# Optimization experiments

Hardware: AMD Instinct MI355X
Metric: run time of the kernel (lower is better)

## Reference

```python
import jax, jax.numpy as jnp
import numpy as np

INPUT_SIZE = 1024
HIDDEN_SIZE = 1024
BATCH = 8192
MLP_H1, MLP_H2 = 16, 8


def _uniform(key, shape, stdv):
    return jax.random.uniform(key, shape, jnp.float32, -stdv, stdv)


def setup_inputs() -> dict:
    key = jax.random.key(0)
    ks = jax.random.split(key, 20)
    stdv = 1.0 / np.sqrt(HIDDEN_SIZE)
    I, H = INPUT_SIZE, HIDDEN_SIZE
    inp = {
        "x": jax.random.normal(ks[0], (BATCH, I), jnp.float32),
        "h": jax.random.normal(ks[1], (BATCH, H), jnp.float32),
        "c": jax.random.normal(ks[2], (BATCH, H), jnp.float32),
        # gate weights (torch layout: matmul(h, W_h*) + matmul(x, W_x*) + b)
        "W_hi": _uniform(ks[3], (H, H), stdv),
        "W_xi": _uniform(ks[4], (I, H), stdv),
        "b_i": _uniform(ks[5], (H,), stdv),
        "W_hc": _uniform(ks[6], (H, H), stdv),
        "W_xc": _uniform(ks[7], (I, H), stdv),
        "b_c": _uniform(ks[8], (H,), stdv),
        "W_ho": _uniform(ks[9], (H, H), stdv),
        "W_xo": _uniform(ks[10], (I, H), stdv),
        "b_o": _uniform(ks[11], (H,), stdv),
        # forget MLP: (I+H) -> 16 -> 8 -> H, ReLU hidden, sigmoid output
        "W1": _uniform(ks[12], (I + H, MLP_H1), stdv),
        "b1": _uniform(ks[13], (MLP_H1,), stdv),
        "W2": _uniform(ks[14], (MLP_H1, MLP_H2), stdv),
        "b2": _uniform(ks[15], (MLP_H2,), stdv),
        "W3": _uniform(ks[16], (MLP_H2, H), stdv),
        "b3": _uniform(ks[17], (H,), stdv),
    }
    return inp


def reference(x, h, c, W_hi, W_xi, b_i, W_hc, W_xc, b_c, W_ho, W_xo, b_o,
              W1, b1, W2, b2, W3, b3):
    # forget gate via small MLP on concat(x, h)
    xh = jnp.concatenate((x, h), axis=1)           # [B, I+H]
    z = jax.nn.relu(xh @ W1 + b1)                  # [B, 16]
    z = jax.nn.relu(z @ W2 + b2)                   # [B, 8]
    f = jax.nn.sigmoid(z @ W3 + b3)                # [B, H]

    i = jax.nn.sigmoid(h @ W_hi + x @ W_xi + b_i)
    g = jnp.tanh(h @ W_hc + x @ W_xc + b_c)
    o = jax.nn.sigmoid(h @ W_ho + x @ W_xo + b_o)

    c_new = f * c + i * g
    h_new = o * jnp.tanh(c_new)
    return (h_new, c_new, f)
```

## Files before the change

### kernel.cpp

```cpp
#include <hip/hip_runtime.h>
#include <math.h>

#define BATCH 8192
#define HDIM  1024
#define KDIM  2048
#define NDIM  3072

typedef __attribute__((ext_vector_type(8))) short short8;
typedef __attribute__((ext_vector_type(4))) float floatx4;

__device__ __forceinline__ float b2f(unsigned short u) {
  union { unsigned int i; float f; } v; v.i = ((unsigned int)u) << 16; return v.f;
}
__device__ __forceinline__ unsigned short f2b(float f) {
  union { unsigned int i; float f; } v; v.f = f;
  unsigned int r = v.i + 0x7FFFu + ((v.i >> 16) & 1u);
  return (unsigned short)(r >> 16);
}
__device__ __forceinline__ float ldsel(const void* p, size_t i, int isbf) {
  return isbf ? b2f(((const unsigned short*)p)[i]) : ((const float*)p)[i];
}
__device__ __forceinline__ float sigf(float x) { return 1.0f / (1.0f + __expf(-x)); }
__device__ __forceinline__ float tanhfast(float x) {
  float a = __builtin_fabsf(x);
  float t = __expf(-2.f * a);
  float r = (1.f - t) / (1.f + t);
  return copysignf(r, x);
}

__device__ __forceinline__ int detect_bf(const void* x) {
  unsigned int w = ((const unsigned int*)x)[threadIdx.x & 63];
  unsigned short lo = (unsigned short)(w & 0xFFFFu);
  int e = (lo >> 7) & 0xFF;
  bool ok = (e >= 110 && e <= 135) || ((lo & 0x7FFFu) == 0);
  unsigned long long m = __ballot(ok);
  return (__popcll(m) >= 48) ? 1 : 0;
}

__device__ __forceinline__ void gld16(const void* g, void* l) {
  auto gp = reinterpret_cast<__attribute__((address_space(1))) unsigned int*>(
      (unsigned long long)g);
  auto lp = reinterpret_cast<__attribute__((address_space(3))) unsigned int*>(
      (unsigned long long)l);
  __builtin_amdgcn_global_load_lds(gp, lp, 16, 0, 0);
}

__device__ __forceinline__ short8 ld8bf(const void* p, size_t off, int isbf) {
  short8 r;
  if (isbf) {
    r = *(const short8*)((const unsigned short*)p + off);
  } else {
    const float* s = (const float*)p + off;
    float4 a = *(const float4*)(s);
    float4 b = *(const float4*)(s + 4);
    r[0]=(short)f2b(a.x); r[1]=(short)f2b(a.y); r[2]=(short)f2b(a.z); r[3]=(short)f2b(a.w);
    r[4]=(short)f2b(b.x); r[5]=(short)f2b(b.y); r[6]=(short)f2b(b.z); r[7]=(short)f2b(b.w);
  }
  return r;
}

__global__ __launch_bounds__(256) void k_prep(
    const void* __restrict__ x, const void* __restrict__ h,
    const void* __restrict__ W1, const void* __restrict__ b1,
    const void* __restrict__ W2, const void* __restrict__ b2,
    unsigned short* __restrict__ A, float* __restrict__ z2) {
  __shared__ __align__(16) unsigned short tA[16 * 256];
  __shared__ __align__(16) unsigned short tB[16 * 256];
  __shared__ float part[4 * 16 * 17];
  __shared__ float z1s[16 * 17];
  const int isbf = detect_bf(x);
  const int tid = threadIdx.x;
  const int m0 = blockIdx.x * 16;
  const int lane = tid & 63;
  const int w = tid >> 6;
  const int q = lane >> 4;
  const int r = lane & 15;
  char* tAb = (char*)tA;
  char* tBb = (char*)tB;

  const int arow = tid >> 4;
  const int ak = (tid & 15) * 16;

  floatx4 acc = {0.f, 0.f, 0.f, 0.f};

  for (int ktile = 0; ktile < 8; ++ktile) {
    const int k0 = ktile * 256;
    const void* src = (k0 < 1024) ? x : h;
    const int klocal = (k0 & 1023) + ak;
    short8 v0 = ld8bf(src, (size_t)(m0 + arow) * 1024 + klocal, isbf);
    short8 v1 = ld8bf(src, (size_t)(m0 + arow) * 1024 + klocal + 8, isbf);
    float wv[16];
    if (isbf) {
      const unsigned short* s = (const unsigned short*)W1 + (size_t)(k0 + tid) * 16;
      short8 s0 = *(const short8*)(s);
      short8 s1 = *(const short8*)(s + 8);
#pragma unroll
      for (int j = 0; j < 8; ++j) { wv[j] = b2f((unsigned short)s0[j]);
                                    wv[8 + j] = b2f((unsigned short)s1[j]); }
    } else {
      const float* s = (const float*)W1 + (size_t)(k0 + tid) * 16;
      float4 a0 = *(const float4*)(s);
      float4 a1 = *(const float4*)(s + 4);
      float4 a2 = *(const float4*)(s + 8);
      float4 a3 = *(const float4*)(s + 12);
      wv[0]=a0.x; wv[1]=a0.y; wv[2]=a0.z; wv[3]=a0.w;
      wv[4]=a1.x; wv[5]=a1.y; wv[6]=a1.z; wv[7]=a1.w;
      wv[8]=a2.x; wv[9]=a2.y; wv[10]=a2.z; wv[11]=a2.w;
      wv[12]=a3.x; wv[13]=a3.y; wv[14]=a3.z; wv[15]=a3.w;
    }
    if (!isbf) {
      unsigned short* Ao = A + (size_t)(m0 + arow) * KDIM + k0 + ak;
      *(short8*)(Ao) = v0;
      *(short8*)(Ao + 8) = v1;
    }
    {
      const int base = arow * 512 + ak * 2;
      const int sw = (arow & 7) << 4;
      *(short8*)(tAb + ((base) ^ sw)) = v0;
      *(short8*)(tAb + ((base + 16) ^ sw)) = v1;
    }
#pragma unroll
    for (int j = 0; j < 16; ++j) {
      *(unsigned short*)(tBb + ((j * 512 + tid * 2) ^ ((j & 7) << 4))) = f2b(wv[j]);
    }
    __syncthreads();
#pragma unroll
    for (int s = 0; s < 2; ++s) {
      const int ks = (w * 2 + s) * 32 + q * 8;
      short8 af = *(const short8*)(tAb + ((r * 512 + ks * 2) ^ ((r & 7) << 4)));
      short8 bf = *(const short8*)(tBb + ((r * 512 + ks * 2) ^ ((r & 7) << 4)));
      acc = __builtin_amdgcn_mfma_f32_16x16x32_bf16(af, bf, acc, 0, 0, 0);
    }
    __syncthreads();
  }
#pragma unroll
  for (int t = 0; t < 4; ++t) part[(w * 16 + q * 4 + t) * 17 + r] = acc[t];
  __syncthreads();
  {
    const int row = tid >> 4;
    const int n = tid & 15;
    float s = part[(0 * 16 + row) * 17 + n] + part[(1 * 16 + row) * 17 + n] +
              part[(2 * 16 + row) * 17 + n] + part[(3 * 16 + row) * 17 + n] +
              ldsel(b1, (size_t)n, isbf);
    z1s[row * 17 + n] = fmaxf(s, 0.f);
  }
  __syncthreads();
  if (tid < 128) {
    const int row = tid >> 3;
    const int p = tid & 7;
    float s = ldsel(b2, (size_t)p, isbf);
#pragma unroll
    for (int nn = 0; nn < 16; ++nn)
      s += z1s[row * 17 + nn] * ldsel(W2, (size_t)nn * 8 + p, isbf);
    z2[(size_t)(m0 + row) * 8 + p] = fmaxf(s, 0.f);
  }
}

__global__ __launch_bounds__(256) void k_wt(
    const void* __restrict__ x,
    const void* __restrict__ wxi, const void* __restrict__ whi,
    const void* __restrict__ wxc, const void* __restrict__ whc,
    const void* __restrict__ wxo, const void* __restrict__ who,
    unsigned short* __restrict__ WT) {
  __shared__ __align__(16) float tbuf[64][65];
  const int isbf = detect_bf(x);
  const int tid = threadIdx.x;
  const int b = blockIdx.x;
  const int mat = b >> 8;
  const int rem = b & 255;
  const int ti = rem >> 4;
  const int tj = rem & 15;
  const void* Ws[6] = {wxi, whi, wxc, whc, wxo, who};
  const void* W = Ws[mat];
  const int gt = mat >> 1;
  const int half = mat & 1;
  const int rrow = tid >> 3;
  const int c8 = (tid & 7) * 8;
#pragma unroll
  for (int it = 0; it < 2; ++it) {
    int row = it * 32 + rrow;
    size_t off = (size_t)(ti * 64 + row) * 1024 + tj * 64 + c8;
    if (isbf) {
      const unsigned short* s = (const unsigned short*)W + off;
      ushort4 a = *(const ushort4*)(s);
      ushort4 bv = *(const ushort4*)(s + 4);
      tbuf[row][c8+0]=b2f(a.x);  tbuf[row][c8+1]=b2f(a.y);
      tbuf[row][c8+2]=b2f(a.z);  tbuf[row][c8+3]=b2f(a.w);
      tbuf[row][c8+4]=b2f(bv.x); tbuf[row][c8+5]=b2f(bv.y);
      tbuf[row][c8+6]=b2f(bv.z); tbuf[row][c8+7]=b2f(bv.w);
    } else {
      const float* s = (const float*)W + off;
      float4 a = *(const float4*)(s);
      float4 bv = *(const float4*)(s + 4);
      tbuf[row][c8+0]=a.x;  tbuf[row][c8+1]=a.y;  tbuf[row][c8+2]=a.z;  tbuf[row][c8+3]=a.w;
      tbuf[row][c8+4]=bv.x; tbuf[row][c8+5]=bv.y; tbuf[row][c8+6]=bv.z; tbuf[row][c8+7]=bv.w;
    }
  }
  __syncthreads();
#pragma unroll
  for (int it = 0; it < 2; ++it) {
    int nl = it * 32 + rrow;
    int n = gt * 1024 + tj * 64 + nl;
    int kk = half * 1024 + ti * 64 + c8;
    short8 pk;
#pragma unroll
    for (int i = 0; i < 8; ++i) pk[i] = (short)f2b(tbuf[c8 + i][nl]);
    *(short8*)(WT + (size_t)n * KDIM + kk) = pk;
  }
}

__global__ __launch_bounds__(256, 3) void k_gemm(
    const void* __restrict__ x, const void* __restrict__ h,
    const unsigned short* __restrict__ Apack,
    const unsigned short* __restrict__ WT,
    unsigned short* __restrict__ P) {
  const int isbf = detect_bf(x);
  const unsigned short* Ax = isbf ? (const unsigned short*)x : Apack;
  const unsigned short* Ah = isbf ? (const unsigned short*)h : (Apack + 1024);
  const int sA = isbf ? 1024 : 2048;
  __shared__ __align__(16) unsigned short lA[128 * 64];
  __shared__ __align__(16) unsigned short lB[128 * 64];
  const int tid = threadIdx.x;
  const int lane = tid & 63;
  const int wv = tid >> 6;
  const int wm = (wv >> 1) << 6;
  const int wn = (wv & 1) << 6;
  const int m0 = blockIdx.y << 7;
  const int n0 = blockIdx.x << 7;

  floatx4 acc[4][4];
  const floatx4 fzero = {0.f, 0.f, 0.f, 0.f};
#pragma unroll
  for (int i = 0; i < 4; ++i)
#pragma unroll
    for (int j = 0; j < 4; ++j) acc[i][j] = fzero;

  int rr[4], kk[4];
#pragma unroll
  for (int ps = 0; ps < 4; ++ps) {
    int chunk = ps * 256 + tid;
    rr[ps] = chunk >> 3;
    kk[ps] = (chunk & 7) ^ (rr[ps] & 7);
  }
  const int px0 = (lane >> 4) ^ (lane & 7);
  const int px1 = ((lane >> 4) + 4) ^ (lane & 7);
  const int rowA = wm + (lane & 15);
  const int rowB = wn + (lane & 15);

  for (int kt = 0; kt < KDIM / 64; ++kt) {
    const int k0 = kt * 64;
    const unsigned short* Abase = (k0 < 1024) ? (Ax + k0) : (Ah + (k0 - 1024));
#pragma unroll
    for (int ps = 0; ps < 4; ++ps) {
      const int chunk = ps * 256 + tid;
      gld16(Abase + (size_t)(m0 + rr[ps]) * sA + kk[ps] * 8, lA + chunk * 8);
      gld16(WT + ((size_t)(n0 + rr[ps]) * KDIM + k0 + kk[ps] * 8), lB + chunk * 8);
    }
    __syncthreads();
#pragma unroll
    for (int s = 0; s < 2; ++s) {
      const int px = s ? px1 : px0;
      short8 af[4], bfr[4];
#pragma unroll
      for (int i = 0; i < 4; ++i)
        af[i] = *(const short8*)(lA + ((((rowA + (i << 4)) << 3) + px) << 3));
#pragma unroll
      for (int i = 0; i < 4; ++i)
        bfr[i] = *(const short8*)(lB + ((((rowB + (i << 4)) << 3) + px) << 3));
#pragma unroll
      for (int mi = 0; mi < 4; ++mi)
#pragma unroll
        for (int ni = 0; ni < 4; ++ni)
          acc[mi][ni] = __builtin_amdgcn_mfma_f32_16x16x32_bf16(
              af[mi], bfr[ni], acc[mi][ni], 0, 0, 0);
    }
    __syncthreads();
  }
  const int col = lane & 15;
  const int rq = (lane >> 4) << 2;
#pragma unroll
  for (int mi = 0; mi < 4; ++mi) {
#pragma unroll
    for (int ni = 0; ni < 4; ++ni) {
      const size_t n = (size_t)(n0 + wn + (ni << 4) + col);
#pragma unroll
      for (int t = 0; t < 4; ++t) {
        const size_t m = (size_t)(m0 + wm + (mi << 4) + rq + t);
        P[m * NDIM + n] = f2b(acc[mi][ni][t]);
      }
    }
  }
}

__global__ __launch_bounds__(256) void k_pointwise(
    const unsigned short* __restrict__ P, const void* __restrict__ x,
    const void* __restrict__ cin,
    const void* __restrict__ bi, const void* __restrict__ bc,
    const void* __restrict__ bo, const float* __restrict__ z2,
    const void* __restrict__ W3, const void* __restrict__ b3,
    void* __restrict__ out) {
  const int isbf = detect_bf(x);
  const int tid = threadIdx.x;
  const int n = tid * 4;
  const size_t MH = (size_t)BATCH * HDIM;

  float w3r[8][4], bif[4], bcf[4], bof[4], b3f[4];
  if (isbf) {
#pragma unroll
    for (int j = 0; j < 8; ++j) {
      ushort4 u = *(const ushort4*)((const unsigned short*)W3 + j * 1024 + n);
      w3r[j][0]=b2f(u.x); w3r[j][1]=b2f(u.y); w3r[j][2]=b2f(u.z); w3r[j][3]=b2f(u.w);
    }
    ushort4 u3 = *(const ushort4*)((const unsigned short*)b3 + n);
    b3f[0]=b2f(u3.x); b3f[1]=b2f(u3.y); b3f[2]=b2f(u3.z); b3f[3]=b2f(u3.w);
    ushort4 a = *(const ushort4*)((const unsigned short*)bi + n);
    ushort4 b = *(const ushort4*)((const unsigned short*)bc + n);
    ushort4 d = *(const ushort4*)((const unsigned short*)bo + n);
    bif[0]=b2f(a.x); bif[1]=b2f(a.y); bif[2]=b2f(a.z); bif[3]=b2f(a.w);
    bcf[0]=b2f(b.x); bcf[1]=b2f(b.y); bcf[2]=b2f(b.z); bcf[3]=b2f(b.w);
    bof[0]=b2f(d.x); bof[1]=b2f(d.y); bof[2]=b2f(d.z); bof[3]=b2f(d.w);
  } else {
#pragma unroll
    for (int j = 0; j < 8; ++j) {
      float4 u = *(const float4*)((const float*)W3 + j * 1024 + n);
      w3r[j][0]=u.x; w3r[j][1]=u.y; w3r[j][2]=u.z; w3r[j][3]=u.w;
    }
    float4 u3 = *(const float4*)((const float*)b3 + n);
    b3f[0]=u3.x; b3f[1]=u3.y; b3f[2]=u3.z; b3f[3]=u3.w;
    float4 a = *(const float4*)((const float*)bi + n);
    float4 b = *(const float4*)((const float*)bc + n);
    float4 d = *(const float4*)((const float*)bo + n);
    bif[0]=a.x; bif[1]=a.y; bif[2]=a.z; bif[3]=a.w;
    bcf[0]=b.x; bcf[1]=b.y; bcf[2]=b.z; bcf[3]=b.w;
    bof[0]=d.x; bof[1]=d.y; bof[2]=d.z; bof[3]=d.w;
  }

  const size_t m0 = (size_t)blockIdx.x * 8;
#pragma unroll
  for (int rI = 0; rI < 8; ++rI) {
    const size_t m = m0 + rI;
    const size_t idx = m * 1024 + n;
    const unsigned short* pr = P + m * NDIM + n;
    ushort4 ui = *(const ushort4*)(pr);
    ushort4 ug = *(const ushort4*)(pr + 1024);
    ushort4 uo = *(const ushort4*)(pr + 2048);
    float pi[4] = {b2f(ui.x), b2f(ui.y), b2f(ui.z), b2f(ui.w)};
    float pg[4] = {b2f(ug.x), b2f(ug.y), b2f(ug.z), b2f(ug.w)};
    float po[4] = {b2f(uo.x), b2f(uo.y), b2f(uo.z), b2f(uo.w)};
    float4 za = *(const float4*)(z2 + m * 8);
    float4 zb = *(const float4*)(z2 + m * 8 + 4);
    float zz[8] = {za.x, za.y, za.z, za.w, zb.x, zb.y, zb.z, zb.w};
    float cf[4];
    if (isbf) {
      ushort4 e = *(const ushort4*)((const unsigned short*)cin + idx);
      cf[0]=b2f(e.x); cf[1]=b2f(e.y); cf[2]=b2f(e.z); cf[3]=b2f(e.w);
    } else {
      float4 e = *(const float4*)((const float*)cin + idx);
      cf[0]=e.x; cf[1]=e.y; cf[2]=e.z; cf[3]=e.w;
    }
    float f3[4] = {b3f[0], b3f[1], b3f[2], b3f[3]};
#pragma unroll
    for (int j = 0; j < 8; ++j) {
      f3[0] += zz[j] * w3r[j][0];
      f3[1] += zz[j] * w3r[j][1];
      f3[2] += zz[j] * w3r[j][2];
      f3[3] += zz[j] * w3r[j][3];
    }
    float hn[4], cn[4], ff[4];
#pragma unroll
    for (int t = 0; t < 4; ++t) {
      float F = sigf(f3[t]);
      float I = sigf(pi[t] + bif[t]);
      float G = tanhfast(pg[t] + bcf[t]);
      float O = sigf(po[t] + bof[t]);
      float C = F * cf[t] + I * G;
      ff[t] = F;
      cn[t] = C;
      hn[t] = O * tanhfast(C);
    }
    if (isbf) {
      unsigned short* ob = (unsigned short*)out;
      *(ushort4*)(ob + idx) = make_ushort4(f2b(hn[0]), f2b(hn[1]), f2b(hn[2]), f2b(hn[3]));
      *(ushort4*)(ob + MH + idx) = make_ushort4(f2b(cn[0]), f2b(cn[1]), f2b(cn[2]), f2b(cn[3]));
      *(ushort4*)(ob + 2 * MH + idx) = make_ushort4(f2b(ff[0]), f2b(ff[1]), f2b(ff[2]), f2b(ff[3]));
    } else {
      float* ob = (float*)out;
      *(float4*)(ob + idx) = make_float4(hn[0], hn[1], hn[2], hn[3]);
      *(float4*)(ob + MH + idx) = make_float4(cn[0], cn[1], cn[2], cn[3]);
      *(float4*)(ob + 2 * MH + idx) = make_float4(ff[0], ff[1], ff[2], ff[3]);
    }
  }
}

extern "C" void kernel_launch(void* const* d_in, const int* in_sizes, int n_in,
                              void* d_out, int out_size, void* d_ws, size_t ws_size,
                              hipStream_t stream) {
  const void* x    = d_in[0];
  const void* h    = d_in[1];
  const void* c    = d_in[2];
  const void* W_hi = d_in[3];
  const void* W_xi = d_in[4];
  const void* b_i  = d_in[5];
  const void* W_hc = d_in[6];
  const void* W_xc = d_in[7];
  const void* b_c  = d_in[8];
  const void* W_ho = d_in[9];
  const void* W_xo = d_in[10];
  const void* b_o  = d_in[11];
  const void* W1   = d_in[12];
  const void* b1   = d_in[13];
  const void* W2   = d_in[14];
  const void* b2   = d_in[15];
  const void* W3   = d_in[16];
  const void* b3   = d_in[17];

  char* ws = (char*)d_ws;
  unsigned short* A   = (unsigned short*)ws;
  unsigned short* WT  = (unsigned short*)(ws + 33554432);
  unsigned short* P   = (unsigned short*)(ws + 46137344);
  float*          z2b = (float*)(ws + 96468992);

  k_prep<<<dim3(512), dim3(256), 0, stream>>>(x, h, W1, b1, W2, b2, A, z2b);
  k_wt<<<dim3(1536), dim3(256), 0, stream>>>(x, W_xi, W_hi, W_xc, W_hc,
                                             W_xo, W_ho, WT);
  k_gemm<<<dim3(NDIM / 128, BATCH / 128), dim3(256), 0, stream>>>(x, h, A, WT, P);
  k_pointwise<<<dim3(BATCH / 8), dim3(256), 0, stream>>>(P, x, c, b_i, b_c, b_o,
                                                         z2b, W3, b3, d_out);
}
```

Baseline: 351.2 us.

## Merge prep and weight-transpose kernels, swizzle GEMM tiles, widen pointwise vectors

Folds the MLP-prep and weight-transpose kernels into one launch, picking the path from the block index, so one launch and its dependency gap go away and the two jobs can share the GPU. Remaps GEMM block indices with a stride swizzle to change which tiles run at the same time, aiming for better L2 reuse. The pointwise kernel now handles 8 columns per thread with 16-byte loads and stores over 4 rows per block, and keeps W3 packed as bf16 in registers. In fp32 mode W3 is rounded to bf16, which adds a small precision loss in the forget gate.

```diff
diff --git a/kernel.cpp b/kernel.cpp
--- a/kernel.cpp
+++ b/kernel.cpp
@@ -59,153 +59,164 @@
   return r;
 }
 
-__global__ __launch_bounds__(256) void k_prep(
+__device__ __forceinline__ void ld8f(const void* p, size_t off, int isbf, float* o) {
+  if (isbf) {
+    short8 s = *(const short8*)((const unsigned short*)p + off);
+#pragma unroll
+    for (int j = 0; j < 8; ++j) o[j] = b2f((unsigned short)s[j]);
+  } else {
+    const float* s = (const float*)p + off;
+    float4 a = *(const float4*)(s);
+    float4 b = *(const float4*)(s + 4);
+    o[0]=a.x; o[1]=a.y; o[2]=a.z; o[3]=a.w;
+    o[4]=b.x; o[5]=b.y; o[6]=b.z; o[7]=b.w;
+  }
+}
+
+__global__ __launch_bounds__(256) void k_pre(
     const void* __restrict__ x, const void* __restrict__ h,
     const void* __restrict__ W1, const void* __restrict__ b1,
     const void* __restrict__ W2, const void* __restrict__ b2,
-    unsigned short* __restrict__ A, float* __restrict__ z2) {
-  __shared__ __align__(16) unsigned short tA[16 * 256];
-  __shared__ __align__(16) unsigned short tB[16 * 256];
-  __shared__ float part[4 * 16 * 17];
-  __shared__ float z1s[16 * 17];
-  const int isbf = detect_bf(x);
-  const int tid = threadIdx.x;
-  const int m0 = blockIdx.x * 16;
-  const int lane = tid & 63;
-  const int w = tid >> 6;
-  const int q = lane >> 4;
-  const int r = lane & 15;
-  char* tAb = (char*)tA;
-  char* tBb = (char*)tB;
-
-  const int arow = tid >> 4;
-  const int ak = (tid & 15) * 16;
-
-  floatx4 acc = {0.f, 0.f, 0.f, 0.f};
-
-  for (int ktile = 0; ktile < 8; ++ktile) {
-    const int k0 = ktile * 256;
-    const void* src = (k0 < 1024) ? x : h;
-    const int klocal = (k0 & 1023) + ak;
-    short8 v0 = ld8bf(src, (size_t)(m0 + arow) * 1024 + klocal, isbf);
-    short8 v1 = ld8bf(src, (size_t)(m0 + arow) * 1024 + klocal + 8, isbf);
-    float wv[16];
-    if (isbf) {
-      const unsigned short* s = (const unsigned short*)W1 + (size_t)(k0 + tid) * 16;
-      short8 s0 = *(const short8*)(s);
-      short8 s1 = *(const short8*)(s + 8);
-#pragma unroll
-      for (int j = 0; j < 8; ++j) { wv[j] = b2f((unsigned short)s0[j]);
-                                    wv[8 + j] = b2f((unsigned short)s1[j]); }
-    } else {
-      const float* s = (const float*)W1 + (size_t)(k0 + tid) * 16;
-      float4 a0 = *(const float4*)(s);
-      float4 a1 = *(const float4*)(s + 4);
-      float4 a2 = *(const float4*)(s + 8);
-      float4 a3 = *(const float4*)(s + 12);
-      wv[0]=a0.x; wv[1]=a0.y; wv[2]=a0.z; wv[3]=a0.w;
-      wv[4]=a1.x; wv[5]=a1.y; wv[6]=a1.z; wv[7]=a1.w;
-      wv[8]=a2.x; wv[9]=a2.y; wv[10]=a2.z; wv[11]=a2.w;
-      wv[12]=a3.x; wv[13]=a3.y; wv[14]=a3.z; wv[15]=a3.w;
-    }
-    if (!isbf) {
-      unsigned short* Ao = A + (size_t)(m0 + arow) * KDIM + k0 + ak;
-      *(short8*)(Ao) = v0;
-      *(short8*)(Ao + 8) = v1;
-    }
-    {
-      const int base = arow * 512 + ak * 2;
-      const int sw = (arow & 7) << 4;
-      *(short8*)(tAb + ((base) ^ sw)) = v0;
-      *(short8*)(tAb + ((base + 16) ^ sw)) = v1;
-    }
-#pragma unroll
-    for (int j = 0; j < 16; ++j) {
-      *(unsigned short*)(tBb + ((j * 512 + tid * 2) ^ ((j & 7) << 4))) = f2b(wv[j]);
-    }
-    __syncthreads();
-#pragma unroll
-    for (int s = 0; s < 2; ++s) {
-      const int ks = (w * 2 + s) * 32 + q * 8;
-      short8 af = *(const short8*)(tAb + ((r * 512 + ks * 2) ^ ((r & 7) << 4)));
-      short8 bf = *(const short8*)(tBb + ((r * 512 + ks * 2) ^ ((r & 7) << 4)));
-      acc = __builtin_amdgcn_mfma_f32_16x16x32_bf16(af, bf, acc, 0, 0, 0);
-    }
-    __syncthreads();
-  }
-#pragma unroll
-  for (int t = 0; t < 4; ++t) part[(w * 16 + q * 4 + t) * 17 + r] = acc[t];
-  __syncthreads();
-  {
-    const int row = tid >> 4;
-    const int n = tid & 15;
-    float s = part[(0 * 16 + row) * 17 + n] + part[(1 * 16 + row) * 17 + n] +
-              part[(2 * 16 + row) * 17 + n] + part[(3 * 16 + row) * 17 + n] +
-              ldsel(b1, (size_t)n, isbf);
-    z1s[row * 17 + n] = fmaxf(s, 0.f);
-  }
-  __syncthreads();
-  if (tid < 128) {
-    const int row = tid >> 3;
-    const int p = tid & 7;
-    float s = ldsel(b2, (size_t)p, isbf);
-#pragma unroll
-    for (int nn = 0; nn < 16; ++nn)
-      s += z1s[row * 17 + nn] * ldsel(W2, (size_t)nn * 8 + p, isbf);
-    z2[(size_t)(m0 + row) * 8 + p] = fmaxf(s, 0.f);
-  }
-}
-
-__global__ __launch_bounds__(256) void k_wt(
-    const void* __restrict__ x,
     const void* __restrict__ wxi, const void* __restrict__ whi,
     const void* __restrict__ wxc, const void* __restrict__ whc,
     const void* __restrict__ wxo, const void* __restrict__ who,
-    unsigned short* __restrict__ WT) {
-  __shared__ __align__(16) float tbuf[64][65];
+    unsigned short* __restrict__ A, unsigned short* __restrict__ WT,
+    float* __restrict__ z2) {
+  __shared__ __align__(16) char smem[21888];
   const int isbf = detect_bf(x);
   const int tid = threadIdx.x;
-  const int b = blockIdx.x;
-  const int mat = b >> 8;
-  const int rem = b & 255;
-  const int ti = rem >> 4;
-  const int tj = rem & 15;
-  const void* Ws[6] = {wxi, whi, wxc, whc, wxo, who};
-  const void* W = Ws[mat];
-  const int gt = mat >> 1;
-  const int half = mat & 1;
-  const int rrow = tid >> 3;
-  const int c8 = (tid & 7) * 8;
-#pragma unroll
-  for (int it = 0; it < 2; ++it) {
-    int row = it * 32 + rrow;
-    size_t off = (size_t)(ti * 64 + row) * 1024 + tj * 64 + c8;
-    if (isbf) {
-      const unsigned short* s = (const unsigned short*)W + off;
-      ushort4 a = *(const ushort4*)(s);
-      ushort4 bv = *(const ushort4*)(s + 4);
-      tbuf[row][c8+0]=b2f(a.x);  tbuf[row][c8+1]=b2f(a.y);
-      tbuf[row][c8+2]=b2f(a.z);  tbuf[row][c8+3]=b2f(a.w);
-      tbuf[row][c8+4]=b2f(bv.x); tbuf[row][c8+5]=b2f(bv.y);
-      tbuf[row][c8+6]=b2f(bv.z); tbuf[row][c8+7]=b2f(bv.w);
-    } else {
-      const float* s = (const float*)W + off;
-      float4 a = *(const float4*)(s);
-      float4 bv = *(const float4*)(s + 4);
-      tbuf[row][c8+0]=a.x;  tbuf[row][c8+1]=a.y;  tbuf[row][c8+2]=a.z;  tbuf[row][c8+3]=a.w;
-      tbuf[row][c8+4]=bv.x; tbuf[row][c8+5]=bv.y; tbuf[row][c8+6]=bv.z; tbuf[row][c8+7]=bv.w;
-    }
-  }
-  __syncthreads();
-#pragma unroll
-  for (int it = 0; it < 2; ++it) {
-    int nl = it * 32 + rrow;
-    int n = gt * 1024 + tj * 64 + nl;
-    int kk = half * 1024 + ti * 64 + c8;
-    short8 pk;
-#pragma unroll
-    for (int i = 0; i < 8; ++i) pk[i] = (short)f2b(tbuf[c8 + i][nl]);
-    *(short8*)(WT + (size_t)n * KDIM + kk) = pk;
+  const int bx = blockIdx.x;
+
+  if (bx < 512) {
+    char* tAb = smem;
+    char* tBb = smem + 8192;
+    float* part = (float*)(smem + 16384);
+    float* z1s  = (float*)(smem + 20736);
+    const int m0 = bx * 16;
+    const int lane = tid & 63;
+    const int w = tid >> 6;
+    const int q = lane >> 4;
+    const int r = lane & 15;
+    const int arow = tid >> 4;
+    const int ak = (tid & 15) * 16;
+
+    floatx4 acc = {0.f, 0.f, 0.f, 0.f};
+
+    for (int ktile = 0; ktile < 8; ++ktile) {
+      const int k0 = ktile * 256;
+      const void* src = (k0 < 1024) ? x : h;
+      const int klocal = (k0 & 1023) + ak;
+      short8 v0 = ld8bf(src, (size_t)(m0 + arow) * 1024 + klocal, isbf);
+      short8 v1 = ld8bf(src, (size_t)(m0 + arow) * 1024 + klocal + 8, isbf);
+      float wv[16];
+      if (isbf) {
+        const unsigned short* s = (const unsigned short*)W1 + (size_t)(k0 + tid) * 16;
+        short8 s0 = *(const short8*)(s);
+        short8 s1 = *(const short8*)(s + 8);
+#pragma unroll
+        for (int j = 0; j < 8; ++j) { wv[j] = b2f((unsigned short)s0[j]);
+                                      wv[8 + j] = b2f((unsigned short)s1[j]); }
+      } else {
+        const float* s = (const float*)W1 + (size_t)(k0 + tid) * 16;
+        float4 a0 = *(const float4*)(s);
+        float4 a1 = *(const float4*)(s + 4);
+        float4 a2 = *(const float4*)(s + 8);
+        float4 a3 = *(const float4*)(s + 12);
+        wv[0]=a0.x; wv[1]=a0.y; wv[2]=a0.z; wv[3]=a0.w;
+        wv[4]=a1.x; wv[5]=a1.y; wv[6]=a1.z; wv[7]=a1.w;
+        wv[8]=a2.x; wv[9]=a2.y; wv[10]=a2.z; wv[11]=a2.w;
+        wv[12]=a3.x; wv[13]=a3.y; wv[14]=a3.z; wv[15]=a3.w;
+      }
+      if (!isbf) {
+        unsigned short* Ao = A + (size_t)(m0 + arow) * KDIM + k0 + ak;
+        *(short8*)(Ao) = v0;
+        *(short8*)(Ao + 8) = v1;
+      }
+      {
+        const int base = arow * 512 + ak * 2;
+        const int sw = (arow & 7) << 4;
+        *(short8*)(tAb + ((base) ^ sw)) = v0;
+        *(short8*)(tAb + ((base + 16) ^ sw)) = v1;
+      }
+#pragma unroll
+      for (int j = 0; j < 16; ++j) {
+        *(unsigned short*)(tBb + ((j * 512 + tid * 2) ^ ((j & 7) << 4))) = f2b(wv[j]);
+      }
+      __syncthreads();
+#pragma unroll
+      for (int s = 0; s < 2; ++s) {
+        const int ks = (w * 2 + s) * 32 + q * 8;
+        short8 af = *(const short8*)(tAb + ((r * 512 + ks * 2) ^ ((r & 7) << 4)));
+        short8 bf = *(const short8*)(tBb + ((r * 512 + ks * 2) ^ ((r & 7) << 4)));
+        acc = __builtin_amdgcn_mfma_f32_16x16x32_bf16(af, bf, acc, 0, 0, 0);
+      }
+      __syncthreads();
+    }
+#pragma unroll
+    for (int t = 0; t < 4; ++t) part[(w * 16 + q * 4 + t) * 17 + r] = acc[t];
+    __syncthreads();
+    {
+      const int row = tid >> 4;
+      const int n = tid & 15;
+      float s = part[(0 * 16 + row) * 17 + n] + part[(1 * 16 + row) * 17 + n] +
+                part[(2 * 16 + row) * 17 + n] + part[(3 * 16 + row) * 17 + n] +
+                ldsel(b1, (size_t)n, isbf);
+      z1s[row * 17 + n] = fmaxf(s, 0.f);
+    }
+    __syncthreads();
+    if (tid < 128) {
+      const int row = tid >> 3;
+      const int p = tid & 7;
+      float s = ldsel(b2, (size_t)p, isbf);
+#pragma unroll
+      for (int nn = 0; nn < 16; ++nn)
+        s += z1s[row * 17 + nn] * ldsel(W2, (size_t)nn * 8 + p, isbf);
+      z2[(size_t)(m0 + row) * 8 + p] = fmaxf(s, 0.f);
+    }
+  } else {
+    float (*tbuf)[65] = (float(*)[65])smem;
+    const int b = bx - 512;
+    const int mat = b >> 8;
+    const int rem = b & 255;
+    const int ti = rem >> 4;
+    const int tj = rem & 15;
+    const void* Ws[6] = {wxi, whi, wxc, whc, wxo, who};
+    const void* W = Ws[mat];
+    const int gt = mat >> 1;
+    const int half = mat & 1;
+    const int rrow = tid >> 3;
+    const int c8 = (tid & 7) * 8;
+#pragma unroll
+    for (int it = 0; it < 2; ++it) {
+      int row = it * 32 + rrow;
+      size_t off = (size_t)(ti * 64 + row) * 1024 + tj * 64 + c8;
+      if (isbf) {
+        const unsigned short* s = (const unsigned short*)W + off;
+        ushort4 a = *(const ushort4*)(s);
+        ushort4 bv = *(const ushort4*)(s + 4);
+        tbuf[row][c8+0]=b2f(a.x);  tbuf[row][c8+1]=b2f(a.y);
+        tbuf[row][c8+2]=b2f(a.z);  tbuf[row][c8+3]=b2f(a.w);
+        tbuf[row][c8+4]=b2f(bv.x); tbuf[row][c8+5]=b2f(bv.y);
+        tbuf[row][c8+6]=b2f(bv.z); tbuf[row][c8+7]=b2f(bv.w);
+      } else {
+        const float* s = (const float*)W + off;
+        float4 a = *(const float4*)(s);
+        float4 bv = *(const float4*)(s + 4);
+        tbuf[row][c8+0]=a.x;  tbuf[row][c8+1]=a.y;  tbuf[row][c8+2]=a.z;  tbuf[row][c8+3]=a.w;
+        tbuf[row][c8+4]=bv.x; tbuf[row][c8+5]=bv.y; tbuf[row][c8+6]=bv.z; tbuf[row][c8+7]=bv.w;
+      }
+    }
+    __syncthreads();
+#pragma unroll
+    for (int it = 0; it < 2; ++it) {
+      int nl = it * 32 + rrow;
+      int n = gt * 1024 + tj * 64 + nl;
+      int kk = half * 1024 + ti * 64 + c8;
+      short8 pk;
+#pragma unroll
+      for (int i = 0; i < 8; ++i) pk[i] = (short)f2b(tbuf[c8 + i][nl]);
+      *(short8*)(WT + (size_t)n * KDIM + kk) = pk;
+    }
   }
 }
 
@@ -225,8 +236,10 @@
   const int wv = tid >> 6;
   const int wm = (wv >> 1) << 6;
   const int wn = (wv & 1) << 6;
-  const int m0 = blockIdx.y << 7;
-  const int n0 = blockIdx.x << 7;
+  const int lin = blockIdx.y * 24 + blockIdx.x;
+  const int swz = ((lin & 7) * 192) + (lin >> 3);
+  const int m0 = (swz / 24) << 7;
+  const int n0 = (swz % 24) << 7;
 
   floatx4 acc[4][4];
   const floatx4 fzero = {0.f, 0.f, 0.f, 0.f};
@@ -301,93 +314,82 @@
     void* __restrict__ out) {
   const int isbf = detect_bf(x);
   const int tid = threadIdx.x;
-  const int n = tid * 4;
+  const int n = (tid & 127) * 8;
+  const int rhalf = tid >> 7;
   const size_t MH = (size_t)BATCH * HDIM;
 
-  float w3r[8][4], bif[4], bcf[4], bof[4], b3f[4];
+  short8 w3p[8];
+  float bif[8], bcf[8], bof[8], b3f[8];
   if (isbf) {
 #pragma unroll
+    for (int j = 0; j < 8; ++j)
+      w3p[j] = *(const short8*)((const unsigned short*)W3 + j * 1024 + n);
+  } else {
+#pragma unroll
     for (int j = 0; j < 8; ++j) {
-      ushort4 u = *(const ushort4*)((const unsigned short*)W3 + j * 1024 + n);
-      w3r[j][0]=b2f(u.x); w3r[j][1]=b2f(u.y); w3r[j][2]=b2f(u.z); w3r[j][3]=b2f(u.w);
-    }
-    ushort4 u3 = *(const ushort4*)((const unsigned short*)b3 + n);
-    b3f[0]=b2f(u3.x); b3f[1]=b2f(u3.y); b3f[2]=b2f(u3.z); b3f[3]=b2f(u3.w);
-    ushort4 a = *(const ushort4*)((const unsigned short*)bi + n);
-    ushort4 b = *(const ushort4*)((const unsigned short*)bc + n);
-    ushort4 d = *(const ushort4*)((const unsigned short*)bo + n);
-    bif[0]=b2f(a.x); bif[1]=b2f(a.y); bif[2]=b2f(a.z); bif[3]=b2f(a.w);
-    bcf[0]=b2f(b.x); bcf[1]=b2f(b.y); bcf[2]=b2f(b.z); bcf[3]=b2f(b.w);
-    bof[0]=b2f(d.x); bof[1]=b2f(d.y); bof[2]=b2f(d.z); bof[3]=b2f(d.w);
-  } else {
-#pragma unroll
-    for (int j = 0; j < 8; ++j) {
-      float4 u = *(const float4*)((const float*)W3 + j * 1024 + n);
-      w3r[j][0]=u.x; w3r[j][1]=u.y; w3r[j][2]=u.z; w3r[j][3]=u.w;
-    }
-    float4 u3 = *(const float4*)((const float*)b3 + n);
-    b3f[0]=u3.x; b3f[1]=u3.y; b3f[2]=u3.z; b3f[3]=u3.w;
-    float4 a = *(const float4*)((const float*)bi + n);
-    float4 b = *(const float4*)((const float*)bc + n);
-    float4 d = *(const float4*)((const float*)bo + n);
-    bif[0]=a.x; bif[1]=a.y; bif[2]=a.z; bif[3]=a.w;
-    bcf[0]=b.x; bcf[1]=b.y; bcf[2]=b.z; bcf[3]=b.w;
-    bof[0]=d.x; bof[1]=d.y; bof[2]=d.z; bof[3]=d.w;
-  }
-
-  const size_t m0 = (size_t)blockIdx.x * 8;
-#pragma unroll
-  for (int rI = 0; rI < 8; ++rI) {
-    const size_t m = m0 + rI;
-    const size_t idx = m * 1024 + n;
+      const float* s = (const float*)W3 + j * 1024 + n;
+      float4 a = *(const float4*)(s);
+      float4 b = *(const float4*)(s + 4);
+      short8 pk;
+      pk[0]=(short)f2b(a.x); pk[1]=(short)f2b(a.y); pk[2]=(short)f2b(a.z); pk[3]=(short)f2b(a.w);
+      pk[4]=(short)f2b(b.x); pk[5]=(short)f2b(b.y); pk[6]=(short)f2b(b.z); pk[7]=(short)f2b(b.w);
+      w3p[j] = pk;
+    }
+  }
+  ld8f(bi, (size_t)n, isbf, bif);
+  ld8f(bc, (size_t)n, isbf, bcf);
+  ld8f(bo, (size_t)n, isbf, bof);
+  ld8f(b3, (size_t)n, isbf, b3f);
+
+  const size_t mbase = (size_t)blockIdx.x * 4 + rhalf;
+#pragma unroll
+  for (int rI = 0; rI < 2; ++rI) {
+    const size_t m = mbase + rI * 2;
+    const size_t idx = m * HDIM + n;
     const unsigned short* pr = P + m * NDIM + n;
-    ushort4 ui = *(const ushort4*)(pr);
-    ushort4 ug = *(const ushort4*)(pr + 1024);
-    ushort4 uo = *(const ushort4*)(pr + 2048);
-    float pi[4] = {b2f(ui.x), b2f(ui.y), b2f(ui.z), b2f(ui.w)};
-    float pg[4] = {b2f(ug.x), b2f(ug.y), b2f(ug.z), b2f(ug.w)};
-    float po[4] = {b2f(uo.x), b2f(uo.y), b2f(uo.z), b2f(uo.w)};
+    short8 ui = *(const short8*)(pr);
+    short8 ug = *(const short8*)(pr + 1024);
+    short8 uo = *(const short8*)(pr + 2048);
     float4 za = *(const float4*)(z2 + m * 8);
     float4 zb = *(const float4*)(z2 + m * 8 + 4);
     float zz[8] = {za.x, za.y, za.z, za.w, zb.x, zb.y, zb.z, zb.w};
-    float cf[4];
-    if (isbf) {
-      ushort4 e = *(const ushort4*)((const unsigned short*)cin + idx);
-      cf[0]=b2f(e.x); cf[1]=b2f(e.y); cf[2]=b2f(e.z); cf[3]=b2f(e.w);
-    } else {
-      float4 e = *(const float4*)((const float*)cin + idx);
-      cf[0]=e.x; cf[1]=e.y; cf[2]=e.z; cf[3]=e.w;
-    }
-    float f3[4] = {b3f[0], b3f[1], b3f[2], b3f[3]};
-#pragma unroll
-    for (int j = 0; j < 8; ++j) {
-      f3[0] += zz[j] * w3r[j][0];
-      f3[1] += zz[j] * w3r[j][1];
-      f3[2] += zz[j] * w3r[j][2];
-      f3[3] += zz[j] * w3r[j][3];
-    }
-    float hn[4], cn[4], ff[4];
-#pragma unroll
-    for (int t = 0; t < 4; ++t) {
-      float F = sigf(f3[t]);
-      float I = sigf(pi[t] + bif[t]);
-      float G = tanhfast(pg[t] + bcf[t]);
-      float O = sigf(po[t] + bof[t]);
-      float C = F * cf[t] + I * G;
+    float cf[8];
+    ld8f(cin, idx, isbf, cf);
+    float hn[8], cn[8], ff[8];
+#pragma unroll
+    for (int t = 0; t < 8; ++t) {
+      float f3 = b3f[t];
+#pragma unroll
+      for (int j = 0; j < 8; ++j) f3 += zz[j] * b2f((unsigned short)w3p[j][t]);
+      const float F = sigf(f3);
+      const float I = sigf(b2f((unsigned short)ui[t]) + bif[t]);
+      const float G = tanhfast(b2f((unsigned short)ug[t]) + bcf[t]);
+      const float O = sigf(b2f((unsigned short)uo[t]) + bof[t]);
+      const float C = F * cf[t] + I * G;
       ff[t] = F;
       cn[t] = C;
       hn[t] = O * tanhfast(C);
     }
     if (isbf) {
       unsigned short* ob = (unsigned short*)out;
-      *(ushort4*)(ob + idx) = make_ushort4(f2b(hn[0]), f2b(hn[1]), f2b(hn[2]), f2b(hn[3]));
-      *(ushort4*)(ob + MH + idx) = make_ushort4(f2b(cn[0]), f2b(cn[1]), f2b(cn[2]), f2b(cn[3]));
-      *(ushort4*)(ob + 2 * MH + idx) = make_ushort4(f2b(ff[0]), f2b(ff[1]), f2b(ff[2]), f2b(ff[3]));
+      short8 ph, pc, pf;
+#pragma unroll
+      for (int t = 0; t < 8; ++t) {
+        ph[t] = (short)f2b(hn[t]);
+        pc[t] = (short)f2b(cn[t]);
+        pf[t] = (short)f2b(ff[t]);
+      }
+      *(short8*)(ob + idx) = ph;
+      *(short8*)(ob + MH + idx) = pc;
+      *(short8*)(ob + 2 * MH + idx) = pf;
     } else {
       float* ob = (float*)out;
-      *(float4*)(ob + idx) = make_float4(hn[0], hn[1], hn[2], hn[3]);
-      *(float4*)(ob + MH + idx) = make_float4(cn[0], cn[1], cn[2], cn[3]);
-      *(float4*)(ob + 2 * MH + idx) = make_float4(ff[0], ff[1], ff[2], ff[3]);
+      *(float4*)(ob + idx)     = make_float4(hn[0], hn[1], hn[2], hn[3]);
+      *(float4*)(ob + idx + 4) = make_float4(hn[4], hn[5], hn[6], hn[7]);
+      *(float4*)(ob + MH + idx)     = make_float4(cn[0], cn[1], cn[2], cn[3]);
+      *(float4*)(ob + MH + idx + 4) = make_float4(cn[4], cn[5], cn[6], cn[7]);
+      *(float4*)(ob + 2 * MH + idx)     = make_float4(ff[0], ff[1], ff[2], ff[3]);
+      *(float4*)(ob + 2 * MH + idx + 4) = make_float4(ff[4], ff[5], ff[6], ff[7]);
     }
   }
 }
@@ -420,10 +422,10 @@
   unsigned short* P   = (unsigned short*)(ws + 46137344);
   float*          z2b = (float*)(ws + 96468992);
 
-  k_prep<<<dim3(512), dim3(256), 0, stream>>>(x, h, W1, b1, W2, b2, A, z2b);
-  k_wt<<<dim3(1536), dim3(256), 0, stream>>>(x, W_xi, W_hi, W_xc, W_hc,
-                                             W_xo, W_ho, WT);
+  k_pre<<<dim3(2048), dim3(256), 0, stream>>>(x, h, W1, b1, W2, b2,
+                                              W_xi, W_hi, W_xc, W_hc, W_xo, W_ho,
+                                              A, WT, z2b);
   k_gemm<<<dim3(NDIM / 128, BATCH / 128), dim3(256), 0, stream>>>(x, h, A, WT, P);
-  k_pointwise<<<dim3(BATCH / 8), dim3(256), 0, stream>>>(P, x, c, b_i, b_c, b_o,
+  k_pointwise<<<dim3(BATCH / 4), dim3(256), 0, stream>>>(P, x, c, b_i, b_c, b_o,
                                                          z2b, W3, b3, d_out);
 }
```

Result: slower. 364.4 us (+3.8%).
